# Kernel optimization log

Hardware: AMD Instinct MI355X
Metric: run time of the kernel (lower is better)

Reference implementation:

```python
import jax, jax.numpy as jnp
import numpy as np

N = 50000
E = 800000
IN = 128
HID = 64
HEADS = 4
OUT = 128
NEG_SLOPE = 0.2


def _segment_softmax(logits, seg, num_segments):
    # logits: (E, H), seg: (E,) destination node ids
    m = jax.ops.segment_max(logits, seg, num_segments=num_segments)
    m = jnp.where(jnp.isfinite(m), m, 0.0)
    e = jnp.exp(logits - m[seg])
    s = jax.ops.segment_sum(e, seg, num_segments=num_segments)
    return e / (s[seg] + 1e-16)


def _gat_conv(x, edge_index, W, att_src, att_dst, bias, heads, out_ch, concat):
    # PyG GATConv with add_self_loops=True, negative_slope=0.2 (eval mode: no dropout)
    n = x.shape[0]
    loops = jnp.arange(n, dtype=edge_index.dtype)
    src = jnp.concatenate([edge_index[0], loops])
    dst = jnp.concatenate([edge_index[1], loops])
    h = (x @ W).reshape(n, heads, out_ch)                      # (N, H, C)
    a_src = jnp.einsum('nhc,hc->nh', h, att_src)               # (N, H)
    a_dst = jnp.einsum('nhc,hc->nh', h, att_dst)
    logits = jax.nn.leaky_relu(a_src[src] + a_dst[dst], NEG_SLOPE)  # (E', H)
    alpha = _segment_softmax(logits, dst, n)                   # (E', H)
    msg = alpha[:, :, None] * h[src]                           # (E', H, C)
    out = jax.ops.segment_sum(msg, dst, num_segments=n)        # (N, H, C)
    if concat:
        out = out.reshape(n, heads * out_ch)
    else:
        out = out.mean(axis=1)
    return out + bias


def setup_inputs() -> dict:
    key = jax.random.key(0)
    ks = jax.random.split(key, 16)
    hc = HID * HEADS
    s = 0.1
    return {
        'x': jax.random.normal(ks[0], (N, IN), dtype=jnp.float32),
        'edge_index': jax.random.randint(ks[1], (2, E), 0, N, dtype=jnp.int64),
        'W1': jax.random.normal(ks[2], (IN, hc), dtype=jnp.float32) * s,
        'att_src1': jax.random.normal(ks[3], (HEADS, HID), dtype=jnp.float32) * s,
        'att_dst1': jax.random.normal(ks[4], (HEADS, HID), dtype=jnp.float32) * s,
        'b1': jnp.zeros((hc,), dtype=jnp.float32),
        'lin1_w': jax.random.normal(ks[5], (IN, hc), dtype=jnp.float32) * s,
        'lin1_b': jnp.zeros((hc,), dtype=jnp.float32),
        'W2': jax.random.normal(ks[6], (hc, OUT), dtype=jnp.float32) * s,
        'att_src2': jax.random.normal(ks[7], (1, OUT), dtype=jnp.float32) * s,
        'att_dst2': jax.random.normal(ks[8], (1, OUT), dtype=jnp.float32) * s,
        'b2': jnp.zeros((OUT,), dtype=jnp.float32),
        'lin2_w': jax.random.normal(ks[9], (hc, OUT), dtype=jnp.float32) * s,
        'lin2_b': jnp.zeros((OUT,), dtype=jnp.float32),
    }


def reference(x, edge_index, W1, att_src1, att_dst1, b1, lin1_w, lin1_b,
              W2, att_src2, att_dst2, b2, lin2_w, lin2_b):
    # h1 = ELU(GATConv1(x) + Linear1(x))  (dropout is eval-mode no-op)
    h = _gat_conv(x, edge_index, W1, att_src1, att_dst1, b1, HEADS, HID, True)
    h = jax.nn.elu(h + x @ lin1_w + lin1_b)
    # out = GATConv2(h) + Linear2(h)
    o = _gat_conv(h, edge_index, W2, att_src2, att_dst2, b2, 1, OUT, False)
    return o + h @ lin2_w + lin2_b
```

## Files before the change

### kernel.cpp

```cpp
#include <hip/hip_runtime.h>
#include <math.h>

#define N_NODES 50000
#define N_EDGES 800000
#define EP (N_EDGES + N_NODES)
#define IN_CH 128
#define HID 64
#define HEADS 4
#define HC (HID * HEADS)
#define OUT_CH 128
#define NEG_SLOPE 0.2f
#define NSCAN ((N_NODES + 255) / 256)
#define MTILES (N_NODES / 16)

typedef __bf16 bf16x8 __attribute__((ext_vector_type(8)));
typedef float  f32x4  __attribute__((ext_vector_type(4)));

__device__ __forceinline__ float bf2f(unsigned short u) {
    return __uint_as_float(((unsigned)u) << 16);
}
__device__ __forceinline__ unsigned short f2bf(float f) {
    unsigned u = __float_as_uint(f);
    return (unsigned short)((u + 0x7fffu + ((u >> 16) & 1u)) >> 16);
}
__device__ __forceinline__ float2 bf2f2(ushort2 q) {
    return make_float2(bf2f(q.x), bf2f(q.y));
}
__device__ __forceinline__ float lrelu(float v) {
    return v > 0.f ? v : NEG_SLOPE * v;
}
__device__ __forceinline__ bf16x8 ldfrag(const unsigned short* p) {
    uint4 u = *(const uint4*)p;
    return __builtin_bit_cast(bf16x8, u);
}

__global__ void hist_kernel(const int* __restrict__ ei, int* __restrict__ cnt) {
    int e = blockIdx.x * 256 + threadIdx.x;
    if (e >= EP) return;
    int d = (e < N_EDGES) ? ei[N_EDGES + e] : e - N_EDGES;
    atomicAdd(&cnt[d], 1);
}

__global__ void scan1_kernel(const int* __restrict__ cnt,
                             int* __restrict__ row, int* __restrict__ bsum) {
    __shared__ int buf[256];
    int i = blockIdx.x * 256 + threadIdx.x;
    int v = (i < N_NODES) ? cnt[i] : 0;
    buf[threadIdx.x] = v;
    __syncthreads();
#pragma unroll
    for (int off = 1; off < 256; off <<= 1) {
        int t = (threadIdx.x >= off) ? buf[threadIdx.x - off] : 0;
        __syncthreads();
        buf[threadIdx.x] += t;
        __syncthreads();
    }
    if (i < N_NODES) row[i] = buf[threadIdx.x] - v;
    if (threadIdx.x == 255) bsum[blockIdx.x] = buf[255];
}

__global__ void scan2_kernel(const int* __restrict__ bsum,
                             int* __restrict__ boff, int* __restrict__ rowN) {
    __shared__ int buf[256];
    int tid = threadIdx.x;
    int v = (tid < NSCAN) ? bsum[tid] : 0;
    buf[tid] = v;
    __syncthreads();
#pragma unroll
    for (int off = 1; off < 256; off <<= 1) {
        int t = (tid >= off) ? buf[tid - off] : 0;
        __syncthreads();
        buf[tid] += t;
        __syncthreads();
    }
    if (tid < NSCAN) boff[tid] = buf[tid] - v;
    if (tid == 255) rowN[0] = buf[255];
}

__global__ void scan3_kernel(int* __restrict__ row, const int* __restrict__ boff,
                             int* __restrict__ pos) {
    int i = blockIdx.x * 256 + threadIdx.x;
    if (i >= N_NODES) return;
    int r = row[i] + boff[blockIdx.x];
    row[i] = r;
    pos[i] = r;
}

__global__ void scatter_kernel(const int* __restrict__ ei,
                               int* __restrict__ pos, int* __restrict__ adjS) {
    int e = blockIdx.x * 256 + threadIdx.x;
    if (e >= EP) return;
    int s, d;
    if (e < N_EDGES) { s = ei[e]; d = ei[N_EDGES + e]; }
    else             { s = d = e - N_EDGES; }
    int p = atomicAdd(&pos[d], 1);
    adjS[p] = s;
}

__global__ void convx_kernel(const float* __restrict__ x,
                             unsigned short* __restrict__ xb) {
    int i = blockIdx.x * 256 + threadIdx.x;
    if (i >= N_NODES * (IN_CH / 4)) return;
    float4 v = ((const float4*)x)[i];
    ushort4 o;
    o.x = f2bf(v.x); o.y = f2bf(v.y); o.z = f2bf(v.z); o.w = f2bf(v.w);
    ((ushort4*)xb)[i] = o;
}

__global__ void pack1_kernel(const float* __restrict__ W1,
                             const float* __restrict__ L1,
                             unsigned short* __restrict__ Bp) {
    int t = blockIdx.x * 256 + threadIdx.x;
    if (t >= 128 * 64) return;
    int frag = t >> 6, l = t & 63;
    int ks = frag >> 5, nf = frag & 31;
    int col = nf * 16 + (l & 15);
    int kb = ks * 32 + (l >> 4) * 8;
    unsigned short* o = Bp + (size_t)t * 8;
#pragma unroll
    for (int i = 0; i < 8; ++i) {
        int k = kb + i;
        float v = (col < HC) ? W1[k * HC + col] : L1[k * HC + (col - HC)];
        o[i] = f2bf(v);
    }
}

__global__ void pack2_kernel(const float* __restrict__ W2,
                             const float* __restrict__ L2,
                             unsigned short* __restrict__ Bp) {
    int t = blockIdx.x * 256 + threadIdx.x;
    if (t >= 128 * 64) return;
    int frag = t >> 6, l = t & 63;
    int ks = frag >> 4, nf = frag & 15;
    int col = nf * 16 + (l & 15);
    int kb = ks * 32 + (l >> 4) * 8;
    unsigned short* o = Bp + (size_t)t * 8;
#pragma unroll
    for (int i = 0; i < 8; ++i) {
        int k = kb + i;
        float v = (col < OUT_CH) ? W2[k * OUT_CH + col]
                                 : L2[k * OUT_CH + (col - OUT_CH)];
        o[i] = f2bf(v);
    }
}

__global__ __launch_bounds__(256) void gemm1_mfma(
        const unsigned short* __restrict__ xb,
        const unsigned short* __restrict__ Bp,
        unsigned short* __restrict__ H1b, float* __restrict__ XL1) {
    int m0 = blockIdx.x * 16;
    int w = threadIdx.x >> 6, l = threadIdx.x & 63;
    int row = m0 + (l & 15);
    int koff = (l >> 4) * 8;
    f32x4 acc[8];
#pragma unroll
    for (int f = 0; f < 8; ++f) acc[f] = (f32x4){0.f, 0.f, 0.f, 0.f};
#pragma unroll
    for (int ks = 0; ks < 4; ++ks) {
        bf16x8 a = ldfrag(xb + (size_t)row * IN_CH + ks * 32 + koff);
        const unsigned short* bb = Bp + ((size_t)((ks * 32 + w * 8) * 64 + l)) * 8;
#pragma unroll
        for (int f = 0; f < 8; ++f) {
            bf16x8 b = ldfrag(bb + (size_t)f * 512);
            acc[f] = __builtin_amdgcn_mfma_f32_16x16x32_bf16(a, b, acc[f], 0, 0, 0);
        }
    }
    int rq = (l >> 4) * 4, lc = l & 15;
#pragma unroll
    for (int f = 0; f < 8; ++f) {
        int col = w * 128 + f * 16 + lc;
#pragma unroll
        for (int r = 0; r < 4; ++r) {
            int m = m0 + rq + r;
            float v = acc[f][r];
            if (col < HC) H1b[(size_t)m * HC + col] = f2bf(v);
            else          XL1[(size_t)m * HC + (col - HC)] = v;
        }
    }
}

__global__ __launch_bounds__(256) void gemm2_mfma(
        const unsigned short* __restrict__ HBb,
        const unsigned short* __restrict__ Bp,
        unsigned short* __restrict__ H2b, float* __restrict__ XL2) {
    int m0 = blockIdx.x * 16;
    int w = threadIdx.x >> 6, l = threadIdx.x & 63;
    int row = m0 + (l & 15);
    int koff = (l >> 4) * 8;
    f32x4 acc[4];
#pragma unroll
    for (int f = 0; f < 4; ++f) acc[f] = (f32x4){0.f, 0.f, 0.f, 0.f};
#pragma unroll
    for (int ks = 0; ks < 8; ++ks) {
        bf16x8 a = ldfrag(HBb + (size_t)row * HC + ks * 32 + koff);
        const unsigned short* bb = Bp + ((size_t)((ks * 16 + w * 4) * 64 + l)) * 8;
#pragma unroll
        for (int f = 0; f < 4; ++f) {
            bf16x8 b = ldfrag(bb + (size_t)f * 512);
            acc[f] = __builtin_amdgcn_mfma_f32_16x16x32_bf16(a, b, acc[f], 0, 0, 0);
        }
    }
    int rq = (l >> 4) * 4, lc = l & 15;
#pragma unroll
    for (int f = 0; f < 4; ++f) {
        int col = w * 64 + f * 16 + lc;
#pragma unroll
        for (int r = 0; r < 4; ++r) {
            int m = m0 + rq + r;
            float v = acc[f][r];
            if (col < OUT_CH) H2b[(size_t)m * OUT_CH + col] = f2bf(v);
            else              XL2[(size_t)m * OUT_CH + (col - OUT_CH)] = v;
        }
    }
}

__global__ void att1_kernel(const unsigned short* __restrict__ H1b,
                            const float* __restrict__ as,
                            const float* __restrict__ ad,
                            float* __restrict__ AS, float* __restrict__ AD) {
    int n = blockIdx.x * 4 + (threadIdx.x >> 6);
    int l = threadIdx.x & 63;
    if (n >= N_NODES) return;
    const unsigned short* h = H1b + (size_t)n * HC;
    float vs[HEADS], vd[HEADS];
#pragma unroll
    for (int hh = 0; hh < HEADS; ++hh) {
        float v = bf2f(h[hh * HID + l]);
        vs[hh] = v * as[hh * HID + l];
        vd[hh] = v * ad[hh * HID + l];
    }
#pragma unroll
    for (int off = 32; off; off >>= 1)
#pragma unroll
        for (int hh = 0; hh < HEADS; ++hh) {
            vs[hh] += __shfl_down(vs[hh], off, 64);
            vd[hh] += __shfl_down(vd[hh], off, 64);
        }
    if (l == 0)
#pragma unroll
        for (int hh = 0; hh < HEADS; ++hh) {
            AS[n * HEADS + hh] = vs[hh];
            AD[n * HEADS + hh] = vd[hh];
        }
}

__global__ void att2_kernel(const unsigned short* __restrict__ H2b,
                            const float* __restrict__ as2,
                            const float* __restrict__ ad2,
                            float* __restrict__ AS, float* __restrict__ AD) {
    int n = blockIdx.x * 4 + (threadIdx.x >> 6);
    int l = threadIdx.x & 63;
    if (n >= N_NODES) return;
    const unsigned short* h = H2b + (size_t)n * OUT_CH;
    float v0 = bf2f(h[l]), v1 = bf2f(h[64 + l]);
    float vs = v0 * as2[l] + v1 * as2[64 + l];
    float vd = v0 * ad2[l] + v1 * ad2[64 + l];
#pragma unroll
    for (int off = 32; off; off >>= 1) {
        vs += __shfl_down(vs, off, 64);
        vd += __shfl_down(vd, off, 64);
    }
    if (l == 0) { AS[n] = vs; AD[n] = vd; }
}

__global__ void gather1_kernel(const int* __restrict__ row,
                               const int* __restrict__ adjS,
                               const float* __restrict__ AS,
                               const float* __restrict__ AD,
                               const unsigned short* __restrict__ H1b,
                               const float* __restrict__ XL1,
                               const float* __restrict__ b1,
                               const float* __restrict__ l1b,
                               unsigned short* __restrict__ HBb) {
    int d = blockIdx.x, j = threadIdx.x;
    int hh = j >> 5;
    int beg = row[d], end = row[d + 1];
    float advd = AD[d * HEADS + hh];
    const ushort2* Hr = (const ushort2*)H1b;
    float ax = 0.f, ay = 0.f, esum = 0.f;
    int i = beg;
    for (; i + 4 <= end; i += 4) {
        int s0 = adjS[i], s1 = adjS[i + 1], s2 = adjS[i + 2], s3 = adjS[i + 3];
        float as0 = AS[s0 * HEADS + hh], as1v = AS[s1 * HEADS + hh];
        float as2v = AS[s2 * HEADS + hh], as3v = AS[s3 * HEADS + hh];
        ushort2 q0 = Hr[(size_t)s0 * 128 + j];
        ushort2 q1 = Hr[(size_t)s1 * 128 + j];
        ushort2 q2 = Hr[(size_t)s2 * 128 + j];
        ushort2 q3 = Hr[(size_t)s3 * 128 + j];
        float e0 = expf(lrelu(as0 + advd));
        float e1 = expf(lrelu(as1v + advd));
        float e2 = expf(lrelu(as2v + advd));
        float e3 = expf(lrelu(as3v + advd));
        float2 h0 = bf2f2(q0), h1 = bf2f2(q1), h2 = bf2f2(q2), h3 = bf2f2(q3);
        ax += e0 * h0.x + e1 * h1.x + e2 * h2.x + e3 * h3.x;
        ay += e0 * h0.y + e1 * h1.y + e2 * h2.y + e3 * h3.y;
        esum += e0 + e1 + e2 + e3;
    }
    for (; i < end; ++i) {
        int s = adjS[i];
        float e = expf(lrelu(AS[s * HEADS + hh] + advd));
        float2 hv = bf2f2(Hr[(size_t)s * 128 + j]);
        ax += e * hv.x; ay += e * hv.y; esum += e;
    }
    float inv = 1.f / (esum + 1e-16f);
    float2 xl = ((const float2*)XL1)[(size_t)d * 128 + j];
    float2 bb = ((const float2*)b1)[j];
    float2 lb = ((const float2*)l1b)[j];
    float v0 = ax * inv + xl.x + bb.x + lb.x;
    float v1 = ay * inv + xl.y + bb.y + lb.y;
    v0 = v0 > 0.f ? v0 : expm1f(v0);
    v1 = v1 > 0.f ? v1 : expm1f(v1);
    ((ushort2*)HBb)[(size_t)d * 128 + j] = make_ushort2(f2bf(v0), f2bf(v1));
}

__global__ void gather2_kernel(const int* __restrict__ row,
                               const int* __restrict__ adjS,
                               const float* __restrict__ AS,
                               const float* __restrict__ AD,
                               const unsigned short* __restrict__ H2b,
                               const float* __restrict__ XL2,
                               const float* __restrict__ b2,
                               const float* __restrict__ l2b,
                               float* __restrict__ out) {
    int d = blockIdx.x, l = threadIdx.x;
    int beg = row[d], end = row[d + 1];
    float advd = AD[d];
    const ushort2* Hr = (const ushort2*)H2b;
    float ax = 0.f, ay = 0.f, esum = 0.f;
    int i = beg;
    for (; i + 4 <= end; i += 4) {
        int s0 = adjS[i], s1 = adjS[i + 1], s2 = adjS[i + 2], s3 = adjS[i + 3];
        float as0 = AS[s0], as1v = AS[s1], as2v = AS[s2], as3v = AS[s3];
        ushort2 q0 = Hr[(size_t)s0 * 64 + l];
        ushort2 q1 = Hr[(size_t)s1 * 64 + l];
        ushort2 q2 = Hr[(size_t)s2 * 64 + l];
        ushort2 q3 = Hr[(size_t)s3 * 64 + l];
        float e0 = expf(lrelu(as0 + advd));
        float e1 = expf(lrelu(as1v + advd));
        float e2 = expf(lrelu(as2v + advd));
        float e3 = expf(lrelu(as3v + advd));
        float2 h0 = bf2f2(q0), h1 = bf2f2(q1), h2 = bf2f2(q2), h3 = bf2f2(q3);
        ax += e0 * h0.x + e1 * h1.x + e2 * h2.x + e3 * h3.x;
        ay += e0 * h0.y + e1 * h1.y + e2 * h2.y + e3 * h3.y;
        esum += e0 + e1 + e2 + e3;
    }
    for (; i < end; ++i) {
        int s = adjS[i];
        float e = expf(lrelu(AS[s] + advd));
        float2 hv = bf2f2(Hr[(size_t)s * 64 + l]);
        ax += e * hv.x; ay += e * hv.y; esum += e;
    }
    float inv = 1.f / (esum + 1e-16f);
    float2 xl = ((const float2*)XL2)[(size_t)d * 64 + l];
    float2 bb = ((const float2*)b2)[l];
    float2 lb = ((const float2*)l2b)[l];
    ((float2*)out)[(size_t)d * 64 + l] =
        make_float2(ax * inv + xl.x + bb.x + lb.x,
                    ay * inv + xl.y + bb.y + lb.y);
}

extern "C" void kernel_launch(void* const* d_in, const int* in_sizes, int n_in,
                              void* d_out, int out_size, void* d_ws, size_t ws_size,
                              hipStream_t stream) {
    const float* x    = (const float*)d_in[0];
    const int*   ei   = (const int*)d_in[1];
    const float* W1   = (const float*)d_in[2];
    const float* as1  = (const float*)d_in[3];
    const float* ad1  = (const float*)d_in[4];
    const float* b1   = (const float*)d_in[5];
    const float* l1w  = (const float*)d_in[6];
    const float* l1b  = (const float*)d_in[7];
    const float* W2   = (const float*)d_in[8];
    const float* as2  = (const float*)d_in[9];
    const float* ad2  = (const float*)d_in[10];
    const float* b2   = (const float*)d_in[11];
    const float* l2w  = (const float*)d_in[12];
    const float* l2b  = (const float*)d_in[13];
    float* out = (float*)d_out;

    float* ws = (float*)d_ws;
    unsigned short* xb  = (unsigned short*)ws;
    float* fp = ws + (size_t)N_NODES * 64;
    unsigned short* H1b = (unsigned short*)fp;
    fp += (size_t)N_NODES * 128;
    float* XL1 = fp;
    fp += (size_t)N_NODES * HC;
    unsigned short* HBb = (unsigned short*)fp;
    fp += (size_t)N_NODES * 128;
    float* AS1 = fp; fp += (size_t)N_NODES * HEADS;
    float* AD1 = fp; fp += (size_t)N_NODES * HEADS;
    float* AS2 = fp; fp += N_NODES;
    float* AD2 = fp; fp += N_NODES;
    unsigned short* Bp1 = (unsigned short*)fp; fp += 32768;
    unsigned short* Bp2 = (unsigned short*)fp; fp += 32768;
    int* cnt  = (int*)fp;
    int* row  = cnt + N_NODES;
    int* pos  = row + N_NODES + 1;
    int* bsum = pos + N_NODES;
    int* boff = bsum + NSCAN;
    int* adjS = boff + NSCAN;
    unsigned short* H2b = H1b;
    float* XL2 = XL1;

    int nE = (EP + 255) / 256;

    hipMemsetAsync(cnt, 0, N_NODES * 4, stream);
    hist_kernel<<<nE, 256, 0, stream>>>(ei, cnt);
    scan1_kernel<<<NSCAN, 256, 0, stream>>>(cnt, row, bsum);
    scan2_kernel<<<1, 256, 0, stream>>>(bsum, boff, row + N_NODES);
    scan3_kernel<<<NSCAN, 256, 0, stream>>>(row, boff, pos);
    scatter_kernel<<<nE, 256, 0, stream>>>(ei, pos, adjS);

    convx_kernel<<<(N_NODES * (IN_CH / 4) + 255) / 256, 256, 0, stream>>>(x, xb);
    pack1_kernel<<<(128 * 64 + 255) / 256, 256, 0, stream>>>(W1, l1w, Bp1);
    pack2_kernel<<<(128 * 64 + 255) / 256, 256, 0, stream>>>(W2, l2w, Bp2);

    gemm1_mfma<<<MTILES, 256, 0, stream>>>(xb, Bp1, H1b, XL1);
    att1_kernel<<<(N_NODES + 3) / 4, 256, 0, stream>>>(H1b, as1, ad1, AS1, AD1);
    gather1_kernel<<<N_NODES, 128, 0, stream>>>(row, adjS, AS1, AD1, H1b, XL1,
                                                b1, l1b, HBb);

    gemm2_mfma<<<MTILES, 256, 0, stream>>>(HBb, Bp2, H2b, XL2);
    att2_kernel<<<(N_NODES + 3) / 4, 256, 0, stream>>>(H2b, as2, ad2, AS2, AD2);
    gather2_kernel<<<N_NODES, 64, 0, stream>>>(row, adjS, AS2, AD2, H2b, XL2,
                                               b2, l2b, out);
}
```

Measured before the change: 324.3 us.

## Precompute per-edge attention exponentials in separate kernels and widen gather1 vectors

Adds el1/el2 kernels that compute exp(leaky_relu(a_src+a_dst)) once per edge and head into a buffer, using a new destination array that the scatter kernel now writes. The gather kernels then read those precomputed weights instead of doing the exp and the AS gather per lane. gather1 also moves to 64 threads per block, each loading ushort4 (four channels). This removes redundant exp and AS loads per lane, but adds two extra launches, extra buffer writes and reads (about 3.4M floats for layer 1), and lower per-block parallelism in gather1.

Measured after the change: 333.9 us. 1.03x slower.

```diff
diff --git a/kernel.cpp b/kernel.cpp
--- a/kernel.cpp
+++ b/kernel.cpp
@@ -23,9 +23,6 @@
     unsigned u = __float_as_uint(f);
     return (unsigned short)((u + 0x7fffu + ((u >> 16) & 1u)) >> 16);
 }
-__device__ __forceinline__ float2 bf2f2(ushort2 q) {
-    return make_float2(bf2f(q.x), bf2f(q.y));
-}
 __device__ __forceinline__ float lrelu(float v) {
     return v > 0.f ? v : NEG_SLOPE * v;
 }
@@ -87,7 +84,8 @@
 }
 
 __global__ void scatter_kernel(const int* __restrict__ ei,
-                               int* __restrict__ pos, int* __restrict__ adjS) {
+                               int* __restrict__ pos,
+                               int* __restrict__ adjS, int* __restrict__ adjD) {
     int e = blockIdx.x * 256 + threadIdx.x;
     if (e >= EP) return;
     int s, d;
@@ -95,6 +93,7 @@
     else             { s = d = e - N_EDGES; }
     int p = atomicAdd(&pos[d], 1);
     adjS[p] = s;
+    adjD[p] = d;
 }
 
 __global__ void convx_kernel(const float* __restrict__ x,
@@ -263,60 +262,84 @@
     if (l == 0) { AS[n] = vs; AD[n] = vd; }
 }
 
+__global__ void el1_kernel(const int* __restrict__ adjS,
+                           const int* __restrict__ adjD,
+                           const float* __restrict__ AS,
+                           const float* __restrict__ AD,
+                           float* __restrict__ EL) {
+    int idx = blockIdx.x * 256 + threadIdx.x;
+    if (idx >= HEADS * EP) return;
+    int h = idx / EP, p = idx - h * EP;
+    int s = adjS[p], d = adjD[p];
+    EL[idx] = expf(lrelu(AS[s * HEADS + h] + AD[d * HEADS + h]));
+}
+
+__global__ void el2_kernel(const int* __restrict__ adjS,
+                           const int* __restrict__ adjD,
+                           const float* __restrict__ AS,
+                           const float* __restrict__ AD,
+                           float* __restrict__ EL) {
+    int p = blockIdx.x * 256 + threadIdx.x;
+    if (p >= EP) return;
+    EL[p] = expf(lrelu(AS[adjS[p]] + AD[adjD[p]]));
+}
+
 __global__ void gather1_kernel(const int* __restrict__ row,
                                const int* __restrict__ adjS,
-                               const float* __restrict__ AS,
-                               const float* __restrict__ AD,
+                               const float* __restrict__ EL,
                                const unsigned short* __restrict__ H1b,
                                const float* __restrict__ XL1,
                                const float* __restrict__ b1,
                                const float* __restrict__ l1b,
                                unsigned short* __restrict__ HBb) {
     int d = blockIdx.x, j = threadIdx.x;
-    int hh = j >> 5;
+    int hh = j >> 4;
     int beg = row[d], end = row[d + 1];
-    float advd = AD[d * HEADS + hh];
-    const ushort2* Hr = (const ushort2*)H1b;
-    float ax = 0.f, ay = 0.f, esum = 0.f;
+    const float* ELh = EL + (size_t)hh * EP;
+    const ushort4* Hr = (const ushort4*)H1b;
+    float a0 = 0.f, a1 = 0.f, a2 = 0.f, a3 = 0.f, esum = 0.f;
     int i = beg;
     for (; i + 4 <= end; i += 4) {
         int s0 = adjS[i], s1 = adjS[i + 1], s2 = adjS[i + 2], s3 = adjS[i + 3];
-        float as0 = AS[s0 * HEADS + hh], as1v = AS[s1 * HEADS + hh];
-        float as2v = AS[s2 * HEADS + hh], as3v = AS[s3 * HEADS + hh];
-        ushort2 q0 = Hr[(size_t)s0 * 128 + j];
-        ushort2 q1 = Hr[(size_t)s1 * 128 + j];
-        ushort2 q2 = Hr[(size_t)s2 * 128 + j];
-        ushort2 q3 = Hr[(size_t)s3 * 128 + j];
-        float e0 = expf(lrelu(as0 + advd));
-        float e1 = expf(lrelu(as1v + advd));
-        float e2 = expf(lrelu(as2v + advd));
-        float e3 = expf(lrelu(as3v + advd));
-        float2 h0 = bf2f2(q0), h1 = bf2f2(q1), h2 = bf2f2(q2), h3 = bf2f2(q3);
-        ax += e0 * h0.x + e1 * h1.x + e2 * h2.x + e3 * h3.x;
-        ay += e0 * h0.y + e1 * h1.y + e2 * h2.y + e3 * h3.y;
+        float e0 = ELh[i], e1 = ELh[i + 1], e2 = ELh[i + 2], e3 = ELh[i + 3];
+        ushort4 q0 = Hr[(size_t)s0 * 64 + j];
+        ushort4 q1 = Hr[(size_t)s1 * 64 + j];
+        ushort4 q2 = Hr[(size_t)s2 * 64 + j];
+        ushort4 q3 = Hr[(size_t)s3 * 64 + j];
+        a0 += e0 * bf2f(q0.x) + e1 * bf2f(q1.x) + e2 * bf2f(q2.x) + e3 * bf2f(q3.x);
+        a1 += e0 * bf2f(q0.y) + e1 * bf2f(q1.y) + e2 * bf2f(q2.y) + e3 * bf2f(q3.y);
+        a2 += e0 * bf2f(q0.z) + e1 * bf2f(q1.z) + e2 * bf2f(q2.z) + e3 * bf2f(q3.z);
+        a3 += e0 * bf2f(q0.w) + e1 * bf2f(q1.w) + e2 * bf2f(q2.w) + e3 * bf2f(q3.w);
         esum += e0 + e1 + e2 + e3;
     }
     for (; i < end; ++i) {
         int s = adjS[i];
-        float e = expf(lrelu(AS[s * HEADS + hh] + advd));
-        float2 hv = bf2f2(Hr[(size_t)s * 128 + j]);
-        ax += e * hv.x; ay += e * hv.y; esum += e;
+        float e = ELh[i];
+        ushort4 q = Hr[(size_t)s * 64 + j];
+        a0 += e * bf2f(q.x); a1 += e * bf2f(q.y);
+        a2 += e * bf2f(q.z); a3 += e * bf2f(q.w);
+        esum += e;
     }
     float inv = 1.f / (esum + 1e-16f);
-    float2 xl = ((const float2*)XL1)[(size_t)d * 128 + j];
-    float2 bb = ((const float2*)b1)[j];
-    float2 lb = ((const float2*)l1b)[j];
-    float v0 = ax * inv + xl.x + bb.x + lb.x;
-    float v1 = ay * inv + xl.y + bb.y + lb.y;
+    float4 xl = ((const float4*)XL1)[(size_t)d * 64 + j];
+    float4 bb = ((const float4*)b1)[j];
+    float4 lb = ((const float4*)l1b)[j];
+    float v0 = a0 * inv + xl.x + bb.x + lb.x;
+    float v1 = a1 * inv + xl.y + bb.y + lb.y;
+    float v2 = a2 * inv + xl.z + bb.z + lb.z;
+    float v3 = a3 * inv + xl.w + bb.w + lb.w;
     v0 = v0 > 0.f ? v0 : expm1f(v0);
     v1 = v1 > 0.f ? v1 : expm1f(v1);
-    ((ushort2*)HBb)[(size_t)d * 128 + j] = make_ushort2(f2bf(v0), f2bf(v1));
+    v2 = v2 > 0.f ? v2 : expm1f(v2);
+    v3 = v3 > 0.f ? v3 : expm1f(v3);
+    ushort4 o;
+    o.x = f2bf(v0); o.y = f2bf(v1); o.z = f2bf(v2); o.w = f2bf(v3);
+    ((ushort4*)HBb)[(size_t)d * 64 + j] = o;
 }
 
 __global__ void gather2_kernel(const int* __restrict__ row,
                                const int* __restrict__ adjS,
-                               const float* __restrict__ AS,
-                               const float* __restrict__ AD,
+                               const float* __restrict__ EL,
                                const unsigned short* __restrict__ H2b,
                                const float* __restrict__ XL2,
                                const float* __restrict__ b2,
@@ -324,31 +347,26 @@
                                float* __restrict__ out) {
     int d = blockIdx.x, l = threadIdx.x;
     int beg = row[d], end = row[d + 1];
-    float advd = AD[d];
     const ushort2* Hr = (const ushort2*)H2b;
     float ax = 0.f, ay = 0.f, esum = 0.f;
     int i = beg;
     for (; i + 4 <= end; i += 4) {
         int s0 = adjS[i], s1 = adjS[i + 1], s2 = adjS[i + 2], s3 = adjS[i + 3];
-        float as0 = AS[s0], as1v = AS[s1], as2v = AS[s2], as3v = AS[s3];
+        float e0 = EL[i], e1 = EL[i + 1], e2 = EL[i + 2], e3 = EL[i + 3];
         ushort2 q0 = Hr[(size_t)s0 * 64 + l];
         ushort2 q1 = Hr[(size_t)s1 * 64 + l];
         ushort2 q2 = Hr[(size_t)s2 * 64 + l];
         ushort2 q3 = Hr[(size_t)s3 * 64 + l];
-        float e0 = expf(lrelu(as0 + advd));
-        float e1 = expf(lrelu(as1v + advd));
-        float e2 = expf(lrelu(as2v + advd));
-        float e3 = expf(lrelu(as3v + advd));
-        float2 h0 = bf2f2(q0), h1 = bf2f2(q1), h2 = bf2f2(q2), h3 = bf2f2(q3);
-        ax += e0 * h0.x + e1 * h1.x + e2 * h2.x + e3 * h3.x;
-        ay += e0 * h0.y + e1 * h1.y + e2 * h2.y + e3 * h3.y;
+        ax += e0 * bf2f(q0.x) + e1 * bf2f(q1.x) + e2 * bf2f(q2.x) + e3 * bf2f(q3.x);
+        ay += e0 * bf2f(q0.y) + e1 * bf2f(q1.y) + e2 * bf2f(q2.y) + e3 * bf2f(q3.y);
         esum += e0 + e1 + e2 + e3;
     }
     for (; i < end; ++i) {
         int s = adjS[i];
-        float e = expf(lrelu(AS[s] + advd));
-        float2 hv = bf2f2(Hr[(size_t)s * 64 + l]);
-        ax += e * hv.x; ay += e * hv.y; esum += e;
+        float e = EL[i];
+        ushort2 q = Hr[(size_t)s * 64 + l];
+        ax += e * bf2f(q.x); ay += e * bf2f(q.y);
+        esum += e;
     }
     float inv = 1.f / (esum + 1e-16f);
     float2 xl = ((const float2*)XL2)[(size_t)d * 64 + l];
@@ -391,6 +409,7 @@
     float* AD1 = fp; fp += (size_t)N_NODES * HEADS;
     float* AS2 = fp; fp += N_NODES;
     float* AD2 = fp; fp += N_NODES;
+    float* EL1 = fp; fp += (size_t)HEADS * EP;
     unsigned short* Bp1 = (unsigned short*)fp; fp += 32768;
     unsigned short* Bp2 = (unsigned short*)fp; fp += 32768;
     int* cnt  = (int*)fp;
@@ -399,8 +418,10 @@
     int* bsum = pos + N_NODES;
     int* boff = bsum + NSCAN;
     int* adjS = boff + NSCAN;
+    int* adjD = adjS + EP;
     unsigned short* H2b = H1b;
     float* XL2 = XL1;
+    float* EL2 = EL1;
 
     int nE = (EP + 255) / 256;
 
@@ -409,7 +430,7 @@
     scan1_kernel<<<NSCAN, 256, 0, stream>>>(cnt, row, bsum);
     scan2_kernel<<<1, 256, 0, stream>>>(bsum, boff, row + N_NODES);
     scan3_kernel<<<NSCAN, 256, 0, stream>>>(row, boff, pos);
-    scatter_kernel<<<nE, 256, 0, stream>>>(ei, pos, adjS);
+    scatter_kernel<<<nE, 256, 0, stream>>>(ei, pos, adjS, adjD);
 
     convx_kernel<<<(N_NODES * (IN_CH / 4) + 255) / 256, 256, 0, stream>>>(x, xb);
     pack1_kernel<<<(128 * 64 + 255) / 256, 256, 0, stream>>>(W1, l1w, Bp1);
@@ -417,11 +438,13 @@
 
     gemm1_mfma<<<MTILES, 256, 0, stream>>>(xb, Bp1, H1b, XL1);
     att1_kernel<<<(N_NODES + 3) / 4, 256, 0, stream>>>(H1b, as1, ad1, AS1, AD1);
-    gather1_kernel<<<N_NODES, 128, 0, stream>>>(row, adjS, AS1, AD1, H1b, XL1,
-                                                b1, l1b, HBb);
+    el1_kernel<<<(HEADS * EP + 255) / 256, 256, 0, stream>>>(adjS, adjD, AS1, AD1, EL1);
+    gather1_kernel<<<N_NODES, 64, 0, stream>>>(row, adjS, EL1, H1b, XL1,
+                                               b1, l1b, HBb);
 
     gemm2_mfma<<<MTILES, 256, 0, stream>>>(HBb, Bp2, H2b, XL2);
     att2_kernel<<<(N_NODES + 3) / 4, 256, 0, stream>>>(H2b, as2, ad2, AS2, AD2);
-    gather2_kernel<<<N_NODES, 64, 0, stream>>>(row, adjS, AS2, AD2, H2b, XL2,
+    el2_kernel<<<nE, 256, 0, stream>>>(adjS, adjD, AS2, AD2, EL2);
+    gather2_kernel<<<N_NODES, 64, 0, stream>>>(row, adjS, EL2, H2b, XL2,
                                                b2, l2b, out);
 }
```
